# Kernel tuning notes

Measured on AMD Instinct MI355X. Metric: run time of the kernel, lower is better.

## Reference

```python
import jax, jax.numpy as jnp
import numpy as np

W_DIM = 512   # latent dim
CH = 512      # number of Fourier channels / output channels
SIZE = 64     # spatial size (square: size[0]=size[1])
SR = 64.0     # sampling_rate
BW = 2.0      # bandwidth
BATCH = 32


def setup_inputs() -> dict:
    key = jax.random.key(0)
    k1, k2, k3, k4, k5 = jax.random.split(key, 5)
    w = jax.random.normal(k1, (BATCH, W_DIM), jnp.float32)
    # affine FC params (weight_init=0 in original; use small random so t varies)
    affine_w = jax.random.normal(k2, (4, W_DIM), jnp.float32) * 0.1
    affine_b = jnp.array([1.0, 0.0, 0.0, 0.0], jnp.float32)
    # channel-mixing weight
    weight = jax.random.normal(k3, (CH, CH), jnp.float32)
    # freqs buffer init: randn, normalized by r*exp(r^2/4), scaled by bandwidth
    f = jax.random.normal(k4, (CH, 2), jnp.float32)
    radii = jnp.sqrt(jnp.sum(f * f, axis=1, keepdims=True))
    f = f / (radii * jnp.exp(radii * radii / 4.0)) * BW
    phases = jax.random.uniform(k5, (CH,), jnp.float32) - 0.5
    return {"w": w, "affine_w": affine_w, "affine_b": affine_b,
            "weight": weight, "freqs": f, "phases": phases}


def reference(w, affine_w, affine_b, weight, freqs, phases):
    # affine FC: FullyConnectedLayer with lr_multiplier=1 -> weight_gain = 1/sqrt(in)
    gain = np.float32(1.0 / np.sqrt(W_DIM))
    t = w @ (affine_w.T * gain) + affine_b                      # [N, 4]
    t = t / jnp.linalg.norm(t[:, :2], axis=1, keepdims=True)
    c, s, tx, ty = t[:, 0], t[:, 1], t[:, 2], t[:, 3]
    # combined transform = m_r @ m_t @ I; top-left 2x2 rotation block:
    R = jnp.stack([jnp.stack([c, -s], -1),
                   jnp.stack([s, c], -1)], axis=1)              # [N, 2, 2]
    # translation column of combined transform (m_r @ m_t)[:, :2, 2]
    trans = jnp.stack([-c * tx + s * ty, -s * tx - c * ty], -1) # [N, 2]
    ph = phases[None, :] + jnp.einsum('cd,nd->nc', freqs, trans)  # [N, C]
    fr = jnp.einsum('cd,nde->nce', freqs, R)                      # [N, C, 2]
    amp = jnp.clip(1.0 - (jnp.linalg.norm(fr, axis=2) - BW) / (SR / 2.0 - BW), 0.0, 1.0)  # [N, C]
    # affine_grid(theta, [1,1,H,W], align_corners=False): base coords (2i+1)/D - 1
    scale = np.float32(0.5 * SIZE / SR)
    xs = ((2.0 * jnp.arange(SIZE, dtype=jnp.float32) + 1.0) / SIZE - 1.0) * scale
    ys = ((2.0 * jnp.arange(SIZE, dtype=jnp.float32) + 1.0) / SIZE - 1.0) * scale
    grid = jnp.stack([jnp.broadcast_to(xs[None, :], (SIZE, SIZE)),
                      jnp.broadcast_to(ys[:, None], (SIZE, SIZE))], axis=-1)  # [H, W, 2]
    # per-pixel Fourier phase: [N, H, W, C]
    x = jnp.einsum('hwd,ncd->nhwc', grid, fr) + ph[:, None, None, :]
    x = jnp.sin(x * np.float32(2.0 * np.pi)) * amp[:, None, None, :]
    # channel projection, then to NCHW
    x = jnp.einsum('nhwc,kc->nkhw', x, weight * np.float32(1.0 / np.sqrt(CH)))
    return x  # [N, CH, H, W]
```

## Files before the change

kernel.cpp:

```cpp
#include <hip/hip_runtime.h>
#include <hip/hip_bf16.h>

#define WDIM 512
#define CHN  512
#define NB   32
#define SZ   64
#define MTOT 4096

typedef __attribute__((ext_vector_type(4))) float f32x4;
typedef __attribute__((ext_vector_type(8))) short short8;
typedef __attribute__((ext_vector_type(4))) int   int4v;
typedef __attribute__((ext_vector_type(4))) unsigned int uint4v;

__device__ __forceinline__ unsigned pack_bf(float a, float b) {
    union { __hip_bfloat16 h; unsigned short u; } x, y;
    x.h = __float2bfloat16(a); y.h = __float2bfloat16(b);
    return (unsigned)x.u | ((unsigned)y.u << 16);
}
__device__ __forceinline__ float lo16f(unsigned u) {
    union { unsigned x; float f; } t; t.x = u << 16; return t.f;
}
__device__ __forceinline__ float hi16f(unsigned u) {
    union { unsigned x; float f; } t; t.x = u & 0xffff0000u; return t.f;
}

__device__ __forceinline__ void bar_lgkm() {
    __builtin_amdgcn_sched_barrier(0);
    asm volatile("s_waitcnt lgkmcnt(0)" ::: "memory");
    __builtin_amdgcn_s_barrier();
    __builtin_amdgcn_sched_barrier(0);
}

__global__ __launch_bounds__(512) void prep_kernel(
    const float* __restrict__ win,
    const float* __restrict__ affine_w,
    const float* __restrict__ affine_b,
    const float* __restrict__ freqs,
    const float* __restrict__ phases,
    const float* __restrict__ wsrc,
    unsigned* __restrict__ SCA, unsigned* __restrict__ SCB,
    __hip_bfloat16* __restrict__ wbf)
{
    const int b = blockIdx.x;
    const int tid = threadIdx.x;
    if (b < NB * 64) {
        const int n = b >> 6;
        const int w = b & 63;
        __shared__ float red[8][4];
        __shared__ float par[4];

        float wv = win[n * WDIM + tid];
        float p0 = wv * affine_w[0 * WDIM + tid];
        float p1 = wv * affine_w[1 * WDIM + tid];
        float p2 = wv * affine_w[2 * WDIM + tid];
        float p3 = wv * affine_w[3 * WDIM + tid];
        #pragma unroll
        for (int off = 32; off >= 1; off >>= 1) {
            p0 += __shfl_down(p0, off);
            p1 += __shfl_down(p1, off);
            p2 += __shfl_down(p2, off);
            p3 += __shfl_down(p3, off);
        }
        const int wave = tid >> 6;
        if ((tid & 63) == 0) {
            red[wave][0] = p0; red[wave][1] = p1;
            red[wave][2] = p2; red[wave][3] = p3;
        }
        __syncthreads();
        if (tid == 0) {
            const float gain = 0.04419417382415922f;
            float t[4];
            #pragma unroll
            for (int j = 0; j < 4; ++j) {
                float s = 0.0f;
                #pragma unroll
                for (int v = 0; v < 8; ++v) s += red[v][j];
                t[j] = s * gain + affine_b[j];
            }
            float inv = 1.0f / sqrtf(t[0] * t[0] + t[1] * t[1]);
            float c = t[0] * inv, s = t[1] * inv, tx = t[2] * inv, ty = t[3] * inv;
            par[0] = c;
            par[1] = s;
            par[2] = -c * tx + s * ty;
            par[3] = -s * tx - c * ty;
        }
        __syncthreads();
        const float c_ = par[0], s_ = par[1], tr0 = par[2], tr1 = par[3];
        const int c = tid;
        float fx = freqs[c * 2 + 0], fy = freqs[c * 2 + 1];
        float frx = fx * c_ + fy * s_;
        float fry = -fx * s_ + fy * c_;
        float ph = phases[c] + fx * tr0 + fy * tr1;
        float r = sqrtf(frx * frx + fry * fry);
        float amp = 1.0f - (r - 2.0f) * (1.0f / 30.0f);
        amp = fminf(fmaxf(amp, 0.0f), 1.0f);
        float xs = (float)(2 * w + 1) * (1.0f / 128.0f) - 0.5f;
        size_t idx = ((size_t)(n * 64 + w)) * CHN + c;
        float sA = amp * __builtin_amdgcn_sinf(xs * frx);
        float cA = amp * __builtin_amdgcn_cosf(xs * frx);
        float bb = xs * fry + ph;
        SCA[idx] = pack_bf(sA, cA);
        SCB[idx] = pack_bf(__builtin_amdgcn_sinf(bb), __builtin_amdgcn_cosf(bb));
    } else {
        int i = (b - NB * 64) * 512 + tid;
        wbf[i] = __float2bfloat16(wsrc[i] * 0.04419417382415922f);
    }
}

__global__ __launch_bounds__(256, 2) void fused_kernel(
    const unsigned* __restrict__ SCA, const unsigned* __restrict__ SCB,
    const __hip_bfloat16* __restrict__ wbf,
    float* __restrict__ out)
{
    __shared__ __align__(16) __hip_bfloat16 As[128 * 64];
    __shared__ __align__(16) __hip_bfloat16 Bs[2][256 * 64];

    const int bid  = blockIdx.x;
    const int orig = (bid & 7) * 256 + (bid >> 3);
    const int n  = orig >> 6;
    const int kb = ((orig >> 5) & 1) * 256;
    const int mb = (orig & 31) * 128;
    const int h0 = mb >> 6;

    const int tid = threadIdx.x;
    const int lane = tid & 63;
    const int wid  = tid >> 6;
    const int ln15 = lane & 15;
    const int hi4  = lane >> 4;
    const int wk   = wid * 64;

    const int cc0 = (tid & 7) * 8;
    const int rb  = tid >> 3;

    const unsigned* pA0 = SCA + ((size_t)(n * 64 + rb)) * CHN + cc0;
    const unsigned* pA1 = pA0 + 32 * CHN;
    const unsigned* pB0 = SCB + ((size_t)(n * 64 + h0)) * CHN + cc0;
    const unsigned* pB1 = pB0 + CHN;

    auto stageB = [&](int t) {
        const int c0 = t * 64;
        char* base = (char*)Bs[t & 1];
        #pragma unroll
        for (int u = 0; u < 8; ++u) {
            int unit = u * 256 + tid;
            int row = unit >> 3;
            int cbyte = ((unit & 7) << 4) ^ ((row & 7) << 4);
            const __hip_bfloat16* src = wbf + (size_t)(kb + row) * CHN + c0 + (cbyte >> 1);
            char* ldsbase = base + (u * 256 + (wid << 6)) * 16;
            __builtin_amdgcn_global_load_lds(
                (const __attribute__((address_space(1))) unsigned int*)src,
                (__attribute__((address_space(3))) unsigned int*)ldsbase, 16, 0, 0);
        }
    };

    uint4v A00, A01, A10, A11, B00, B01, B10, B11;
    auto loadT = [&](int c0) {
        A00 = *(const uint4v*)(pA0 + c0); A01 = *(const uint4v*)(pA0 + c0 + 4);
        A10 = *(const uint4v*)(pA1 + c0); A11 = *(const uint4v*)(pA1 + c0 + 4);
        B00 = *(const uint4v*)(pB0 + c0); B01 = *(const uint4v*)(pB0 + c0 + 4);
        B10 = *(const uint4v*)(pB1 + c0); B11 = *(const uint4v*)(pB1 + c0 + 4);
    };

    auto features = [&](int c0) {
        #pragma unroll
        for (int i = 0; i < 4; ++i) {
            int m = rb + i * 32;
            uint4v Aa = (i & 1) ? A10 : A00, Ab = (i & 1) ? A11 : A01;
            uint4v Ba = (i >> 1) ? B10 : B00, Bb = (i >> 1) ? B11 : B01;
            union { __hip_bfloat16 h[8]; int4v v; } t;
            #pragma unroll
            for (int j = 0; j < 4; ++j)
                t.h[j] = __float2bfloat16(
                    lo16f(Aa[j]) * hi16f(Ba[j]) + hi16f(Aa[j]) * lo16f(Ba[j]));
            #pragma unroll
            for (int j = 0; j < 4; ++j)
                t.h[4 + j] = __float2bfloat16(
                    lo16f(Ab[j]) * hi16f(Bb[j]) + hi16f(Ab[j]) * lo16f(Bb[j]));
            *(int4v*)((char*)As + m * 128 + ((cc0 * 2) ^ ((m & 7) << 4))) = t.v;
        }
    };

    f32x4 acc[4][8];
    #pragma unroll
    for (int a = 0; a < 4; ++a)
        #pragma unroll
        for (int b = 0; b < 8; ++b)
            acc[a][b] = (f32x4)0.0f;

    loadT(0);
    stageB(0);
    features(0);
    stageB(1);
    __builtin_amdgcn_sched_barrier(0);
    asm volatile("s_waitcnt lgkmcnt(0)" ::: "memory");
    asm volatile("s_waitcnt vmcnt(8)" ::: "memory");
    __builtin_amdgcn_s_barrier();
    __builtin_amdgcn_sched_barrier(0);

    #pragma unroll 1
    for (int kc = 0; kc < 8; ++kc) {
        const char* bsbase = (const char*)Bs[kc & 1];
        #pragma unroll
        for (int kk = 0; kk < 2; ++kk) {
            short8 wf[4], ff[8];
            #pragma unroll
            for (int ki = 0; ki < 4; ++ki) {
                int row = wk + ki * 16 + ln15;
                wf[ki] = *(const short8*)(bsbase + row * 128 +
                          (((kk * 32 + hi4 * 8) * 2) ^ ((row & 7) << 4)));
            }
            #pragma unroll
            for (int mj = 0; mj < 8; ++mj) {
                int m = mj * 16 + ln15;
                ff[mj] = *(const short8*)((char*)As + m * 128 +
                          (((kk * 32 + hi4 * 8) * 2) ^ ((m & 7) << 4)));
            }
            if (kk == 0 && kc < 7)
                loadT((kc + 1) * 64);
            __builtin_amdgcn_s_setprio(1);
            #pragma unroll
            for (int ki = 0; ki < 4; ++ki)
                #pragma unroll
                for (int mj = 0; mj < 8; ++mj)
                    acc[ki][mj] = __builtin_amdgcn_mfma_f32_16x16x32_bf16(
                        wf[ki], ff[mj], acc[ki][mj], 0, 0, 0);
            __builtin_amdgcn_s_setprio(0);
        }

        bar_lgkm();
        if (kc < 7) features((kc + 1) * 64);
        if (kc < 6) stageB(kc + 2);
        bar_lgkm();
    }

    #pragma unroll
    for (int ki = 0; ki < 4; ++ki) {
        #pragma unroll
        for (int mj = 0; mj < 8; ++mj) {
            int kg = kb + wk + ki * 16 + hi4 * 4;
            int mg = mb + mj * 16 + ln15;
            float* op = out + ((size_t)n * CHN + kg) * MTOT + mg;
            #pragma unroll
            for (int r = 0; r < 4; ++r)
                op[(size_t)r * MTOT] = acc[ki][mj][r];
        }
    }
}

extern "C" void kernel_launch(void* const* d_in, const int* in_sizes, int n_in,
                              void* d_out, int out_size, void* d_ws, size_t ws_size,
                              hipStream_t stream) {
    const float* w        = (const float*)d_in[0];
    const float* affine_w = (const float*)d_in[1];
    const float* affine_b = (const float*)d_in[2];
    const float* weight   = (const float*)d_in[3];
    const float* freqs    = (const float*)d_in[4];
    const float* phases   = (const float*)d_in[5];
    float* out = (float*)d_out;

    char* ws = (char*)d_ws;
    __hip_bfloat16* wbf = (__hip_bfloat16*)(ws);
    unsigned* SCA = (unsigned*)(ws + (1u << 20));
    unsigned* SCB = (unsigned*)(ws + (1u << 20) + (4u << 20));

    prep_kernel<<<NB * 64 + (CHN * CHN) / 512, 512, 0, stream>>>(
        w, affine_w, affine_b, freqs, phases, weight, SCA, SCB, wbf);

    fused_kernel<<<2048, 256, 0, stream>>>(SCA, SCB, wbf, out);
}
```

Measured before the change: 111.3 us.

## Enlarge GEMM block tile to 256x256 with 8 waves and double-buffered feature tiles

Each block now computes a 256-pixel by 256-channel output tile with 512 threads in a 2x4 wave grid, instead of a 128x256 tile with 256 threads. The Fourier feature tile in LDS is double-buffered. Weight staging, next-tile feature loads and feature generation are interleaved with the MFMA phases, with a barrier per half-step. The goal is more reuse per loaded weight tile and better overlap of feature generation with matrix math. The cost is prefetching only one stage ahead, more barriers, and LDS use (about 128KB) that likely limits the CU to one block.

```diff
diff --git a/kernel.cpp b/kernel.cpp
--- a/kernel.cpp
+++ b/kernel.cpp
@@ -22,13 +22,6 @@
 }
 __device__ __forceinline__ float hi16f(unsigned u) {
     union { unsigned x; float f; } t; t.x = u & 0xffff0000u; return t.f;
-}
-
-__device__ __forceinline__ void bar_lgkm() {
-    __builtin_amdgcn_sched_barrier(0);
-    asm volatile("s_waitcnt lgkmcnt(0)" ::: "memory");
-    __builtin_amdgcn_s_barrier();
-    __builtin_amdgcn_sched_barrier(0);
 }
 
 __global__ __launch_bounds__(512) void prep_kernel(
@@ -107,19 +100,20 @@
     }
 }
 
-__global__ __launch_bounds__(256, 2) void fused_kernel(
+__global__ __launch_bounds__(512, 2) void fused_kernel(
     const unsigned* __restrict__ SCA, const unsigned* __restrict__ SCB,
     const __hip_bfloat16* __restrict__ wbf,
     float* __restrict__ out)
 {
-    __shared__ __align__(16) __hip_bfloat16 As[128 * 64];
+    __shared__ __align__(16) __hip_bfloat16 As[2][256 * 64];
     __shared__ __align__(16) __hip_bfloat16 Bs[2][256 * 64];
 
     const int bid  = blockIdx.x;
-    const int orig = (bid & 7) * 256 + (bid >> 3);
-    const int n  = orig >> 6;
-    const int kb = ((orig >> 5) & 1) * 256;
-    const int mb = (orig & 31) * 128;
+    const int orig = (bid & 7) * 128 + (bid >> 3);
+    const int n  = orig >> 5;
+    const int om = orig & 31;
+    const int kb = (om >> 4) * 256;
+    const int mb = (om & 15) * 256;
     const int h0 = mb >> 6;
 
     const int tid = threadIdx.x;
@@ -127,56 +121,56 @@
     const int wid  = tid >> 6;
     const int ln15 = lane & 15;
     const int hi4  = lane >> 4;
-    const int wk   = wid * 64;
+    const int wm   = (wid >> 2) * 128;
+    const int wk   = (wid & 3) * 64;
 
     const int cc0 = (tid & 7) * 8;
     const int rb  = tid >> 3;
 
-    const unsigned* pA0 = SCA + ((size_t)(n * 64 + rb)) * CHN + cc0;
-    const unsigned* pA1 = pA0 + 32 * CHN;
-    const unsigned* pB0 = SCB + ((size_t)(n * 64 + h0)) * CHN + cc0;
-    const unsigned* pB1 = pB0 + CHN;
+    const unsigned* pA = SCA + ((size_t)(n * 64 + rb)) * CHN + cc0;
+    const unsigned* pB = SCB + ((size_t)(n * 64 + h0)) * CHN + cc0;
 
     auto stageB = [&](int t) {
         const int c0 = t * 64;
         char* base = (char*)Bs[t & 1];
         #pragma unroll
-        for (int u = 0; u < 8; ++u) {
-            int unit = u * 256 + tid;
+        for (int u = 0; u < 4; ++u) {
+            int unit = u * 512 + tid;
             int row = unit >> 3;
             int cbyte = ((unit & 7) << 4) ^ ((row & 7) << 4);
             const __hip_bfloat16* src = wbf + (size_t)(kb + row) * CHN + c0 + (cbyte >> 1);
-            char* ldsbase = base + (u * 256 + (wid << 6)) * 16;
+            char* ldsbase = base + (u * 512 + (wid << 6)) * 16;
             __builtin_amdgcn_global_load_lds(
                 (const __attribute__((address_space(1))) unsigned int*)src,
                 (__attribute__((address_space(3))) unsigned int*)ldsbase, 16, 0, 0);
         }
     };
 
-    uint4v A00, A01, A10, A11, B00, B01, B10, B11;
+    uint4v A0, A1, B0[4], B1[4];
     auto loadT = [&](int c0) {
-        A00 = *(const uint4v*)(pA0 + c0); A01 = *(const uint4v*)(pA0 + c0 + 4);
-        A10 = *(const uint4v*)(pA1 + c0); A11 = *(const uint4v*)(pA1 + c0 + 4);
-        B00 = *(const uint4v*)(pB0 + c0); B01 = *(const uint4v*)(pB0 + c0 + 4);
-        B10 = *(const uint4v*)(pB1 + c0); B11 = *(const uint4v*)(pB1 + c0 + 4);
+        A0 = *(const uint4v*)(pA + c0); A1 = *(const uint4v*)(pA + c0 + 4);
+        #pragma unroll
+        for (int i = 0; i < 4; ++i) {
+            B0[i] = *(const uint4v*)(pB + (size_t)i * CHN + c0);
+            B1[i] = *(const uint4v*)(pB + (size_t)i * CHN + c0 + 4);
+        }
     };
 
-    auto features = [&](int c0) {
+    auto features = [&](int t) {
+        char* abase = (char*)As[t & 1];
         #pragma unroll
         for (int i = 0; i < 4; ++i) {
-            int m = rb + i * 32;
-            uint4v Aa = (i & 1) ? A10 : A00, Ab = (i & 1) ? A11 : A01;
-            uint4v Ba = (i >> 1) ? B10 : B00, Bb = (i >> 1) ? B11 : B01;
-            union { __hip_bfloat16 h[8]; int4v v; } t;
+            int m = rb + i * 64;
+            union { __hip_bfloat16 h[8]; int4v v; } tt;
             #pragma unroll
             for (int j = 0; j < 4; ++j)
-                t.h[j] = __float2bfloat16(
-                    lo16f(Aa[j]) * hi16f(Ba[j]) + hi16f(Aa[j]) * lo16f(Ba[j]));
+                tt.h[j] = __float2bfloat16(
+                    lo16f(A0[j]) * hi16f(B0[i][j]) + hi16f(A0[j]) * lo16f(B0[i][j]));
             #pragma unroll
             for (int j = 0; j < 4; ++j)
-                t.h[4 + j] = __float2bfloat16(
-                    lo16f(Ab[j]) * hi16f(Bb[j]) + hi16f(Ab[j]) * lo16f(Bb[j]));
-            *(int4v*)((char*)As + m * 128 + ((cc0 * 2) ^ ((m & 7) << 4))) = t.v;
+                tt.h[4 + j] = __float2bfloat16(
+                    lo16f(A1[j]) * hi16f(B1[i][j]) + hi16f(A1[j]) * lo16f(B1[i][j]));
+            *(int4v*)(abase + m * 128 + ((cc0 * 2) ^ ((m & 7) << 4))) = tt.v;
         }
     };
 
@@ -187,36 +181,44 @@
         for (int b = 0; b < 8; ++b)
             acc[a][b] = (f32x4)0.0f;
 
+    stageB(0);
     loadT(0);
-    stageB(0);
     features(0);
     stageB(1);
+    loadT(64);
     __builtin_amdgcn_sched_barrier(0);
     asm volatile("s_waitcnt lgkmcnt(0)" ::: "memory");
-    asm volatile("s_waitcnt vmcnt(8)" ::: "memory");
     __builtin_amdgcn_s_barrier();
     __builtin_amdgcn_sched_barrier(0);
 
     #pragma unroll 1
-    for (int kc = 0; kc < 8; ++kc) {
-        const char* bsbase = (const char*)Bs[kc & 1];
+    for (int t = 0; t < 8; ++t) {
+        const char* bsb = (const char*)Bs[t & 1];
+        const char* asb = (const char*)As[t & 1];
         #pragma unroll
         for (int kk = 0; kk < 2; ++kk) {
             short8 wf[4], ff[8];
             #pragma unroll
             for (int ki = 0; ki < 4; ++ki) {
                 int row = wk + ki * 16 + ln15;
-                wf[ki] = *(const short8*)(bsbase + row * 128 +
+                wf[ki] = *(const short8*)(bsb + row * 128 +
                           (((kk * 32 + hi4 * 8) * 2) ^ ((row & 7) << 4)));
             }
             #pragma unroll
             for (int mj = 0; mj < 8; ++mj) {
-                int m = mj * 16 + ln15;
-                ff[mj] = *(const short8*)((char*)As + m * 128 +
+                int m = wm + mj * 16 + ln15;
+                ff[mj] = *(const short8*)(asb + m * 128 +
                           (((kk * 32 + hi4 * 8) * 2) ^ ((m & 7) << 4)));
             }
-            if (kk == 0 && kc < 7)
-                loadT((kc + 1) * 64);
+            if (kk == 0) {
+                if (t < 7) { stageB(t + 1); loadT((t + 1) * 64); }
+            } else {
+                if (t < 7) features(t + 1);
+            }
+            __builtin_amdgcn_sched_barrier(0);
+            asm volatile("s_waitcnt lgkmcnt(0)" ::: "memory");
+            __builtin_amdgcn_s_barrier();
+            __builtin_amdgcn_sched_barrier(0);
             __builtin_amdgcn_s_setprio(1);
             #pragma unroll
             for (int ki = 0; ki < 4; ++ki)
@@ -225,12 +227,8 @@
                     acc[ki][mj] = __builtin_amdgcn_mfma_f32_16x16x32_bf16(
                         wf[ki], ff[mj], acc[ki][mj], 0, 0, 0);
             __builtin_amdgcn_s_setprio(0);
-        }
-
-        bar_lgkm();
-        if (kc < 7) features((kc + 1) * 64);
-        if (kc < 6) stageB(kc + 2);
-        bar_lgkm();
+            __builtin_amdgcn_sched_barrier(0);
+        }
     }
 
     #pragma unroll
@@ -238,7 +236,7 @@
         #pragma unroll
         for (int mj = 0; mj < 8; ++mj) {
             int kg = kb + wk + ki * 16 + hi4 * 4;
-            int mg = mb + mj * 16 + ln15;
+            int mg = mb + wm + mj * 16 + ln15;
             float* op = out + ((size_t)n * CHN + kg) * MTOT + mg;
             #pragma unroll
             for (int r = 0; r < 4; ++r)
@@ -266,5 +264,5 @@
     prep_kernel<<<NB * 64 + (CHN * CHN) / 512, 512, 0, stream>>>(
         w, affine_w, affine_b, freqs, phases, weight, SCA, SCB, wbf);
 
-    fused_kernel<<<2048, 256, 0, stream>>>(SCA, SCB, wbf, out);
-}
+    fused_kernel<<<1024, 512, 0, stream>>>(SCA, SCB, wbf, out);
+}
```

Measured after the change: 132.2 us. 1.19x slower.
